# Optimization experiments

Measured on AMD Instinct MI355X. Metric: run time of the kernel, lower is better.

Reference implementation:

```python
import jax, jax.numpy as jnp
import numpy as np

DIM = 768
HEADS = 8
HEAD_DIM = DIM // HEADS  # 96
HIDDEN = 1500
EPS = 1e-5
# Faithful quirk: original divides scores by d = (dim/head_num)**(-0.5)
D_QUIRK = (DIM / HEADS) ** (-0.5)


def setup_inputs() -> dict:
    key = jax.random.key(0)
    ks = jax.random.split(key, 12)
    B, N = 8, 1024
    def lin(k, fan_in, fan_out):
        bound = 1.0 / np.sqrt(fan_in)
        return jax.random.uniform(k, (fan_in, fan_out), jnp.float32, -bound, bound)
    return {
        "x": jax.random.normal(ks[0], (B, N, DIM), jnp.float32),
        "ln_g": jnp.ones((DIM,), jnp.float32),
        "ln_b": jnp.zeros((DIM,), jnp.float32),
        "Wqkv": lin(ks[1], DIM, 3 * DIM),
        "bqkv": jnp.zeros((3 * DIM,), jnp.float32),
        "W0": lin(ks[2], DIM, DIM),
        "b0": jnp.zeros((DIM,), jnp.float32),
        "W1": lin(ks[3], DIM, HIDDEN),
        "b1": jnp.zeros((HIDDEN,), jnp.float32),
        "W2": lin(ks[4], HIDDEN, DIM),
        "b2": jnp.zeros((DIM,), jnp.float32),
    }


def _layer_norm(x, g, b):
    mu = jnp.mean(x, axis=-1, keepdims=True)
    var = jnp.var(x, axis=-1, keepdims=True)
    return (x - mu) * jax.lax.rsqrt(var + EPS) * g + b


def _attention(x, Wqkv, bqkv, W0, b0):
    B, N, C = x.shape
    qkv = x @ Wqkv + bqkv                      # [B,N,3C]
    qkv = qkv.reshape(B, N, 3, HEADS, HEAD_DIM)
    qkv = jnp.transpose(qkv, (2, 0, 3, 1, 4))  # [3,B,H,N,hd]
    q, k, v = qkv[0], qkv[1], qkv[2]
    # Faithful: divide by d = head_dim**(-0.5)  (i.e. multiply by sqrt(head_dim))
    scores = jnp.einsum('bhnd,bhmd->bhnm', q, k) / D_QUIRK
    attn = jax.nn.softmax(scores, axis=-1)
    out = jnp.einsum('bhnm,bhmd->bhnd', attn, v)  # [B,H,N,hd]
    out = jnp.transpose(out, (0, 2, 1, 3)).reshape(B, N, C)
    return out @ W0 + b0


def reference(x, ln_g, ln_b, Wqkv, bqkv, W0, b0, W1, b1, W2, b2):
    y = _layer_norm(x, ln_g, ln_b)
    y = _attention(y, Wqkv, bqkv, W0, b0)
    z = y + x
    k = _layer_norm(z, ln_g, ln_b)  # shared LN params (same module reused)
    k = jax.nn.gelu(k @ W1 + b1, approximate=False) @ W2 + b2
    return z + k
```

## Files before the change

### kernel.cpp

```cpp
#include <hip/hip_runtime.h>
#include <hip/hip_bf16.h>

#define DIM 768
#define HEADS 8
#define HD 96
#define HIDDEN 1500
#define HPAD 1536
#define NB 8
#define NSEQ 1024
#define NTOK (NB * NSEQ)
#define LNEPS 1e-5f
#define ATTN_SCALE 9.797958971132712f

typedef __attribute__((ext_vector_type(4))) float f32x4;
typedef __attribute__((ext_vector_type(8))) __bf16 bf16x8;
typedef __attribute__((ext_vector_type(4))) __bf16 bf16x4;

typedef __attribute__((address_space(1))) const unsigned int GU32;
typedef __attribute__((address_space(3))) unsigned int LU32;

__device__ __forceinline__ void gload16(const void* g, void* l) {
    __builtin_amdgcn_global_load_lds((GU32*)g, (LU32*)l, 16, 0, 0);
}

__device__ __forceinline__ float ldsel(const void* p, size_t i, bool bf) {
    return bf ? __bfloat162float(((const __hip_bfloat16*)p)[i])
              : ((const float*)p)[i];
}

__device__ __forceinline__ float gelu_exact(float x) {
    return 0.5f * x * (1.0f + erff(x * 0.7071067811865476f));
}

__global__ void detect_kernel(const unsigned int* __restrict__ g, int* __restrict__ flag) {
    *flag = (g[0] == 0x3F800000u) ? 0 : 1;
}

template <int INDUAL>
__global__ __launch_bounds__(256) void ln_kernel(const void* __restrict__ x,
                                                 const void* __restrict__ gam,
                                                 const void* __restrict__ bet,
                                                 __bf16* __restrict__ outH,
                                                 __bf16* __restrict__ outL,
                                                 const int* __restrict__ flagp) {
    bool bf = (*flagp != 0);
    int row = blockIdx.x;
    int t = threadIdx.x;
    size_t base = (size_t)row * DIM;
    float v0, v1, v2;
    if (INDUAL) {
        v0 = ldsel(x, base + t, bf);
        v1 = ldsel(x, base + t + 256, bf);
        v2 = ldsel(x, base + t + 512, bf);
    } else {
        const float* xr = (const float*)x + base;
        v0 = xr[t]; v1 = xr[t + 256]; v2 = xr[t + 512];
    }
    float s = v0 + v1 + v2;
    float s2 = v0 * v0 + v1 * v1 + v2 * v2;
    __shared__ float r1[256];
    __shared__ float r2[256];
    r1[t] = s; r2[t] = s2;
    __syncthreads();
    for (int o = 128; o > 0; o >>= 1) {
        if (t < o) { r1[t] += r1[t + o]; r2[t] += r2[t + o]; }
        __syncthreads();
    }
    float mean = r1[0] * (1.0f / DIM);
    float var = r2[0] * (1.0f / DIM) - mean * mean;
    float inv = rsqrtf(var + LNEPS);
    float o0 = (v0 - mean) * inv * ldsel(gam, t, bf)       + ldsel(bet, t, bf);
    float o1 = (v1 - mean) * inv * ldsel(gam, t + 256, bf) + ldsel(bet, t + 256, bf);
    float o2 = (v2 - mean) * inv * ldsel(gam, t + 512, bf) + ldsel(bet, t + 512, bf);
    __bf16 h0 = (__bf16)o0; outH[base + t]       = h0; outL[base + t]       = (__bf16)(o0 - (float)h0);
    __bf16 h1 = (__bf16)o1; outH[base + t + 256] = h1; outL[base + t + 256] = (__bf16)(o1 - (float)h1);
    __bf16 h2 = (__bf16)o2; outH[base + t + 512] = h2; outL[base + t + 512] = (__bf16)(o2 - (float)h2);
}

__global__ __launch_bounds__(256) void wsplit_kernel(const void* __restrict__ W,
                                                     __bf16* __restrict__ WTh,
                                                     __bf16* __restrict__ WTl,
                                                     int K, int N, int Kpad, int Ngrid,
                                                     const int* __restrict__ flagp) {
    bool bf = (*flagp != 0);
    __shared__ float T[32][33];
    int tx = threadIdx.x & 31, ty = threadIdx.x >> 5;
    int k0 = blockIdx.x * 32, n0 = blockIdx.y * 32;
#pragma unroll
    for (int i = 0; i < 4; ++i) {
        int k = k0 + ty + i * 8, n = n0 + tx;
        T[ty + i * 8][tx] = (k < K && n < N) ? ldsel(W, (size_t)k * N + n, bf) : 0.0f;
    }
    __syncthreads();
#pragma unroll
    for (int i = 0; i < 4; ++i) {
        int n = n0 + ty + i * 8, k = k0 + tx;
        if (n < Ngrid && k < Kpad) {
            float v = T[tx][ty + i * 8];
            __bf16 h = (__bf16)v;
            WTh[(size_t)n * Kpad + k] = h;
            WTl[(size_t)n * Kpad + k] = (__bf16)(v - (float)h);
        }
    }
}

template <int ACT, int RES, int OUTMODE>
__global__ __launch_bounds__(256, 2) void gemm_kernel(
    const __bf16* __restrict__ AH, const __bf16* __restrict__ AL,
    const __bf16* __restrict__ BH, const __bf16* __restrict__ BL,
    const void* __restrict__ bias,
    const void* __restrict__ resv, int rstride,
    void* __restrict__ outv, int ostride,
    int K, int Nvalid,
    const int* __restrict__ flagp) {
    bool bf = (*flagp != 0);
    __shared__ __align__(16) __bf16 lds[4 * 8192];
    __bf16* sAH = lds;
    __bf16* sAL = lds + 8192;
    __bf16* sBH = lds + 16384;
    __bf16* sBL = lds + 24576;

    int t = threadIdx.x;
    int lane = t & 63, w = t >> 6;
    int wr = w >> 1, wc = w & 1;
    int lr = lane & 15, kq = lane >> 4;

    int gx = gridDim.x;
    int nwg = gx * gridDim.y;
    int orig = blockIdx.y * gx + blockIdx.x;
    int qq = nwg >> 3, rm = nwg & 7;
    int xcd = orig & 7, loc = orig >> 3;
    int wgid = (xcd < rm ? xcd * (qq + 1) : rm * (qq + 1) + (xcd - rm) * qq) + loc;
    int row0 = (wgid / gx) * 128, col0 = (wgid % gx) * 128;

    size_t asrc[4], bsrc[4];
    int ldst[4];
#pragma unroll
    for (int j = 0; j < 4; ++j) {
        int c = j * 256 + t;
        int rr = c >> 3;
        int kbs = (c & 7) ^ (rr & 7);
        asrc[j] = (size_t)(row0 + rr) * K + kbs * 8;
        bsrc[j] = (size_t)(col0 + rr) * K + kbs * 8;
        ldst[j] = c * 8;
    }

    f32x4 acc[4][4];
#pragma unroll
    for (int mi = 0; mi < 4; ++mi)
#pragma unroll
        for (int ni = 0; ni < 4; ++ni)
            acc[mi][ni] = (f32x4){0.f, 0.f, 0.f, 0.f};

    for (int k0 = 0; k0 < K; k0 += 64) {
        __syncthreads();
#pragma unroll
        for (int j = 0; j < 4; ++j) {
            gload16(AH + asrc[j] + k0, sAH + ldst[j]);
            gload16(AL + asrc[j] + k0, sAL + ldst[j]);
            gload16(BH + bsrc[j] + k0, sBH + ldst[j]);
            gload16(BL + bsrc[j] + k0, sBL + ldst[j]);
        }
        __syncthreads();
#pragma unroll
        for (int s = 0; s < 2; ++s) {
            bf16x8 af_h[4], af_l[4], bt_h[4], bt_l[4];
            int kb = s * 4 + kq;
#pragma unroll
            for (int mi = 0; mi < 4; ++mi) {
                int rowm = wr * 64 + mi * 16 + lr;
                int off = (rowm * 8 + (kb ^ (rowm & 7))) * 8;
                af_h[mi] = *(const bf16x8*)(sAH + off);
                af_l[mi] = *(const bf16x8*)(sAL + off);
            }
#pragma unroll
            for (int ni = 0; ni < 4; ++ni) {
                int rown = wc * 64 + ni * 16 + lr;
                int off = (rown * 8 + (kb ^ (rown & 7))) * 8;
                bt_h[ni] = *(const bf16x8*)(sBH + off);
                bt_l[ni] = *(const bf16x8*)(sBL + off);
            }
            if (!bf) {
#pragma unroll
                for (int mi = 0; mi < 4; ++mi)
#pragma unroll
                    for (int ni = 0; ni < 4; ++ni) {
                        acc[mi][ni] = __builtin_amdgcn_mfma_f32_16x16x32_bf16(af_h[mi], bt_h[ni], acc[mi][ni], 0, 0, 0);
                        acc[mi][ni] = __builtin_amdgcn_mfma_f32_16x16x32_bf16(af_l[mi], bt_h[ni], acc[mi][ni], 0, 0, 0);
                        acc[mi][ni] = __builtin_amdgcn_mfma_f32_16x16x32_bf16(af_h[mi], bt_l[ni], acc[mi][ni], 0, 0, 0);
                    }
            } else {
#pragma unroll
                for (int mi = 0; mi < 4; ++mi)
#pragma unroll
                    for (int ni = 0; ni < 4; ++ni) {
                        acc[mi][ni] = __builtin_amdgcn_mfma_f32_16x16x32_bf16(af_h[mi], bt_h[ni], acc[mi][ni], 0, 0, 0);
                        acc[mi][ni] = __builtin_amdgcn_mfma_f32_16x16x32_bf16(af_l[mi], bt_h[ni], acc[mi][ni], 0, 0, 0);
                    }
            }
        }
    }

    int fr = lane & 15, fq = lane >> 4;
#pragma unroll
    for (int mi = 0; mi < 4; ++mi) {
#pragma unroll
        for (int ni = 0; ni < 4; ++ni) {
            int cc = col0 + wc * 64 + ni * 16 + fr;
#pragma unroll
            for (int j = 0; j < 4; ++j) {
                int rr = row0 + wr * 64 + mi * 16 + fq * 4 + j;
                if (cc < Nvalid) {
                    float cval = acc[mi][ni][j] + ldsel(bias, cc, bf);
                    if (ACT == 1) cval = gelu_exact(cval);
                    if (RES == 1) cval += ldsel(resv, (size_t)rr * rstride + cc, bf);
                    if (RES == 2) cval += ((const float*)resv)[(size_t)rr * rstride + cc];
                    if (OUTMODE == 0) {
                        ((float*)outv)[(size_t)rr * ostride + cc] = cval;
                    } else if (OUTMODE == 1) {
                        if (bf)
                            ((__hip_bfloat16*)outv)[(size_t)rr * ostride + cc] = __float2bfloat16(cval);
                        else
                            ((float*)outv)[(size_t)rr * ostride + cc] = cval;
                    } else {
                        __bf16 hv = (__bf16)cval;
                        ((__bf16*)outv)[(size_t)rr * ostride + cc] = hv;
                        ((__bf16*)outv)[(size_t)NTOK * HPAD + (size_t)rr * ostride + cc] =
                            (__bf16)(cval - (float)hv);
                    }
                } else if (OUTMODE == 2) {
                    ((__bf16*)outv)[(size_t)rr * ostride + cc] = (__bf16)0.0f;
                    ((__bf16*)outv)[(size_t)NTOK * HPAD + (size_t)rr * ostride + cc] = (__bf16)0.0f;
                }
            }
        }
    }
}

__global__ __launch_bounds__(256, 3) void attn_kernel(const float* __restrict__ qkv,
                                                      __bf16* __restrict__ oH,
                                                      __bf16* __restrict__ oL) {
    __shared__ __align__(16) char smem[51200];
    char* Kh_s = smem;
    char* Kl_s = smem + 13312;
    char* Vt_s = smem + 26624;
    char* P_s  = smem + 41984;

    int nwg = gridDim.x * gridDim.y;
    int orig = blockIdx.y * gridDim.x + blockIdx.x;
    int qq = nwg >> 3;
    int wgid = (orig & 7) * qq + (orig >> 3);
    int qt = wgid & 15;
    int bh = wgid >> 4;
    int b = bh >> 3, h = bh & 7;
    int t = threadIdx.x;
    int lane = t & 63, w = t >> 6;
    int r = lane & 15, g = lane >> 4;

    const size_t rs = 3 * DIM;

    bf16x8 qh[3], ql[3];
    {
        const float* qp = qkv + ((size_t)b * NSEQ + qt * 64 + w * 16 + r) * rs + h * HD;
#pragma unroll
        for (int kc = 0; kc < 3; ++kc) {
            f32x4 f0 = *(const f32x4*)(qp + kc * 32 + g * 8);
            f32x4 f1 = *(const f32x4*)(qp + kc * 32 + g * 8 + 4);
#pragma unroll
            for (int j = 0; j < 8; ++j) {
                float f = (j < 4) ? f0[j] : f1[j - 4];
                __bf16 hi = (__bf16)f;
                qh[kc][j] = hi;
                ql[kc][j] = (__bf16)(f - (float)hi);
            }
        }
    }

    f32x4 kreg[6], vreg[8];
    const float* kg0 = qkv + (size_t)b * NSEQ * rs + DIM + h * HD;
    const float* vg0 = qkv + (size_t)b * NSEQ * rs + 2 * DIM + h * HD;
    int vdq = t >> 3, voct = t & 7;

    auto load_kv = [&](int jt) {
        const float* kg = kg0 + (size_t)(jt * 64) * rs;
#pragma unroll
        for (int i = 0; i < 6; ++i) {
            int u = t + i * 256;
            int key = u / 24, dp = u % 24;
            kreg[i] = *(const f32x4*)(kg + (size_t)key * rs + dp * 4);
        }
        if (t < 192) {
            const float* vg = vg0 + (size_t)(jt * 64) * rs;
#pragma unroll
            for (int koff = 0; koff < 8; ++koff)
                vreg[koff] = *(const f32x4*)(vg + (size_t)(voct * 8 + koff) * rs + vdq * 4);
        }
    };

    auto store_kv = [&]() {
#pragma unroll
        for (int i = 0; i < 6; ++i) {
            int u = t + i * 256;
            int key = u / 24, dp = u % 24;
            bf16x4 kh4, kl4;
#pragma unroll
            for (int j = 0; j < 4; ++j) {
                __bf16 hi = (__bf16)kreg[i][j];
                kh4[j] = hi;
                kl4[j] = (__bf16)(kreg[i][j] - (float)hi);
            }
            *(bf16x4*)(Kh_s + key * 208 + dp * 8) = kh4;
            *(bf16x4*)(Kl_s + key * 208 + dp * 8) = kl4;
        }
        if (t < 192) {
#pragma unroll
            for (int j = 0; j < 4; ++j) {
                bf16x8 vrow;
#pragma unroll
                for (int koff = 0; koff < 8; ++koff)
                    vrow[koff] = (__bf16)vreg[koff][j];
                *(bf16x8*)(Vt_s + (vdq * 4 + j) * 160 + voct * 16) = vrow;
            }
        }
    };

    f32x4 o[6];
#pragma unroll
    for (int di = 0; di < 6; ++di) o[di] = (f32x4){0.f, 0.f, 0.f, 0.f};
    float m_i[4], l_i[4];
#pragma unroll
    for (int jj = 0; jj < 4; ++jj) { m_i[jj] = -1e30f; l_i[jj] = 0.0f; }

    load_kv(0);
    for (int jt = 0; jt < NSEQ / 64; ++jt) {
        __syncthreads();
        store_kv();
        __syncthreads();
        if (jt + 1 < NSEQ / 64) load_kv(jt + 1);

        f32x4 sacc[4];
#pragma unroll
        for (int ci = 0; ci < 4; ++ci) sacc[ci] = (f32x4){0.f, 0.f, 0.f, 0.f};
#pragma unroll
        for (int ci = 0; ci < 4; ++ci) {
#pragma unroll
            for (int kc = 0; kc < 3; ++kc) {
                bf16x8 kh = *(const bf16x8*)(Kh_s + (ci * 16 + r) * 208 + kc * 64 + g * 16);
                bf16x8 kl = *(const bf16x8*)(Kl_s + (ci * 16 + r) * 208 + kc * 64 + g * 16);
                sacc[ci] = __builtin_amdgcn_mfma_f32_16x16x32_bf16(qh[kc], kh, sacc[ci], 0, 0, 0);
                sacc[ci] = __builtin_amdgcn_mfma_f32_16x16x32_bf16(ql[kc], kh, sacc[ci], 0, 0, 0);
                sacc[ci] = __builtin_amdgcn_mfma_f32_16x16x32_bf16(qh[kc], kl, sacc[ci], 0, 0, 0);
            }
        }

        float p[4][4];
        float al[4];
#pragma unroll
        for (int jj = 0; jj < 4; ++jj) {
            float s0 = sacc[0][jj] * ATTN_SCALE;
            float s1 = sacc[1][jj] * ATTN_SCALE;
            float s2 = sacc[2][jj] * ATTN_SCALE;
            float s3 = sacc[3][jj] * ATTN_SCALE;
            float mx = fmaxf(fmaxf(s0, s1), fmaxf(s2, s3));
            mx = fmaxf(mx, __shfl_xor(mx, 1));
            mx = fmaxf(mx, __shfl_xor(mx, 2));
            mx = fmaxf(mx, __shfl_xor(mx, 4));
            mx = fmaxf(mx, __shfl_xor(mx, 8));
            float mn = fmaxf(m_i[jj], mx);
            al[jj] = __expf(m_i[jj] - mn);
            p[0][jj] = __expf(s0 - mn);
            p[1][jj] = __expf(s1 - mn);
            p[2][jj] = __expf(s2 - mn);
            p[3][jj] = __expf(s3 - mn);
            float rsm = p[0][jj] + p[1][jj] + p[2][jj] + p[3][jj];
            rsm += __shfl_xor(rsm, 1);
            rsm += __shfl_xor(rsm, 2);
            rsm += __shfl_xor(rsm, 4);
            rsm += __shfl_xor(rsm, 8);
            l_i[jj] = l_i[jj] * al[jj] + rsm;
            m_i[jj] = mn;
        }
#pragma unroll
        for (int di = 0; di < 6; ++di)
#pragma unroll
            for (int jj = 0; jj < 4; ++jj) o[di][jj] *= al[jj];
#pragma unroll
        for (int jj = 0; jj < 4; ++jj)
#pragma unroll
            for (int ci = 0; ci < 4; ++ci)
                ((__bf16*)(P_s + (w * 16 + g * 4 + jj) * 144))[ci * 16 + r] = (__bf16)p[ci][jj];
        asm volatile("" ::: "memory");

        bf16x8 pa[2];
#pragma unroll
        for (int kc2 = 0; kc2 < 2; ++kc2)
            pa[kc2] = *(const bf16x8*)(P_s + (w * 16 + r) * 144 + kc2 * 64 + g * 16);
#pragma unroll
        for (int di = 0; di < 6; ++di) {
#pragma unroll
            for (int kc2 = 0; kc2 < 2; ++kc2) {
                bf16x8 vb = *(const bf16x8*)(Vt_s + (di * 16 + r) * 160 + kc2 * 64 + g * 16);
                o[di] = __builtin_amdgcn_mfma_f32_16x16x32_bf16(pa[kc2], vb, o[di], 0, 0, 0);
            }
        }
    }

    float invl[4];
#pragma unroll
    for (int jj = 0; jj < 4; ++jj) invl[jj] = 1.0f / l_i[jj];
#pragma unroll
    for (int jj = 0; jj < 4; ++jj) {
        size_t tok = (size_t)b * NSEQ + qt * 64 + w * 16 + g * 4 + jj;
        size_t base = tok * DIM + h * HD + r;
#pragma unroll
        for (int di = 0; di < 6; ++di) {
            float v = o[di][jj] * invl[jj];
            __bf16 hv = (__bf16)v;
            oH[base + di * 16] = hv;
            oL[base + di * 16] = (__bf16)(v - (float)hv);
        }
    }
}

extern "C" void kernel_launch(void* const* d_in, const int* in_sizes, int n_in,
                              void* d_out, int out_size, void* d_ws, size_t ws_size,
                              hipStream_t stream) {
    const void* x    = d_in[0];
    const void* ln_g = d_in[1];
    const void* ln_b = d_in[2];
    const void* Wqkv = d_in[3];
    const void* bqkv = d_in[4];
    const void* W0   = d_in[5];
    const void* b0   = d_in[6];
    const void* W1   = d_in[7];
    const void* b1   = d_in[8];
    const void* W2   = d_in[9];
    const void* b2   = d_in[10];

    float* ws = (float*)d_ws;
    __bf16* ylnH = (__bf16*)ws;
    __bf16* ylnL = ylnH + (size_t)NTOK * DIM;
    __bf16* atnH = ylnH;
    __bf16* atnL = ylnL;
    __bf16* klnH = ylnH;
    __bf16* klnL = ylnL;
    float* qkv = ws + (size_t)NTOK * DIM;
    __bf16* r1 = (__bf16*)qkv;
    __bf16* W0Th = r1;
    __bf16* W0Tl = W0Th + (size_t)768 * 768;
    __bf16* W1Th = W0Tl + (size_t)768 * 768;
    __bf16* W1Tl = W1Th + (size_t)HPAD * 768;
    __bf16* W2Th = W1Tl + (size_t)HPAD * 768;
    __bf16* W2Tl = W2Th + (size_t)768 * HPAD;
    __bf16* hH   = W2Tl + (size_t)768 * HPAD;
    __bf16* hL   = hH + (size_t)NTOK * HPAD;
    float* zbuf = ws + (size_t)NTOK * (DIM + 3 * DIM);
    __bf16* WqkvTh = (__bf16*)zbuf;
    __bf16* WqkvTl = WqkvTh + (size_t)(3 * DIM) * DIM;

    int* flag = (int*)(ws + (size_t)NTOK * 3840);

    detect_kernel<<<1, 1, 0, stream>>>((const unsigned int*)ln_g, flag);
    ln_kernel<1><<<NTOK, 256, 0, stream>>>(x, ln_g, ln_b, ylnH, ylnL, flag);
    wsplit_kernel<<<dim3(DIM / 32, (3 * DIM) / 32), 256, 0, stream>>>(
        Wqkv, WqkvTh, WqkvTl, DIM, 3 * DIM, DIM, 3 * DIM, flag);
    gemm_kernel<0, 0, 0><<<dim3((3 * DIM) / 128, NTOK / 128), 256, 0, stream>>>(
        ylnH, ylnL, WqkvTh, WqkvTl, bqkv, nullptr, 0, qkv, 3 * DIM, DIM, 3 * DIM, flag);
    attn_kernel<<<dim3(NSEQ / 64, NB * HEADS), 256, 0, stream>>>(qkv, atnH, atnL);
    wsplit_kernel<<<dim3(DIM / 32, DIM / 32), 256, 0, stream>>>(
        W0, W0Th, W0Tl, DIM, DIM, DIM, DIM, flag);
    wsplit_kernel<<<dim3(DIM / 32, HPAD / 32), 256, 0, stream>>>(
        W1, W1Th, W1Tl, DIM, HIDDEN, DIM, HPAD, flag);
    wsplit_kernel<<<dim3(HPAD / 32, DIM / 32), 256, 0, stream>>>(
        W2, W2Th, W2Tl, HIDDEN, DIM, HPAD, DIM, flag);
    gemm_kernel<0, 1, 0><<<dim3(DIM / 128, NTOK / 128), 256, 0, stream>>>(
        atnH, atnL, W0Th, W0Tl, b0, x, DIM, zbuf, DIM, DIM, DIM, flag);
    ln_kernel<0><<<NTOK, 256, 0, stream>>>(zbuf, ln_g, ln_b, klnH, klnL, flag);
    gemm_kernel<1, 0, 2><<<dim3(HPAD / 128, NTOK / 128), 256, 0, stream>>>(
        klnH, klnL, W1Th, W1Tl, b1, nullptr, 0, hH, HPAD, DIM, HIDDEN, flag);
    gemm_kernel<0, 2, 1><<<dim3(DIM / 128, NTOK / 128), 256, 0, stream>>>(
        hH, hL, W2Th, W2Tl, b2, zbuf, DIM, d_out, DIM, HPAD, DIM, flag);
}
```

Measured before the change: 582.3 us.

## Halve GEMM K-tile, pad V-transpose LDS rows, add lazy softmax rescaling

The GEMM K step drops from 64 to 32 with a new 4-chunk XOR swizzle, halving LDS use per block so more blocks may fit per CU. In attention, the transposed-V row stride grows from 160 to 176 bytes to reduce LDS bank conflicts. The online softmax now rescales the running max and output only when some row's new max exceeds the old one by more than 8, skipping the exponential and multiply work otherwise. In exchange, the GEMM runs twice as many barrier-separated K iterations, and the lazy softmax lets exponentials reach up to e^8 before a rescale, which could overflow bf16 P precision in edge cases.

Result: slower. 655.0 us (+12.5%).

```diff
diff --git a/kernel.cpp b/kernel.cpp
--- a/kernel.cpp
+++ b/kernel.cpp
@@ -114,11 +114,11 @@
     int K, int Nvalid,
     const int* __restrict__ flagp) {
     bool bf = (*flagp != 0);
-    __shared__ __align__(16) __bf16 lds[4 * 8192];
+    __shared__ __align__(16) __bf16 lds[4 * 4096];
     __bf16* sAH = lds;
-    __bf16* sAL = lds + 8192;
-    __bf16* sBH = lds + 16384;
-    __bf16* sBL = lds + 24576;
+    __bf16* sAL = lds + 4096;
+    __bf16* sBH = lds + 8192;
+    __bf16* sBL = lds + 12288;
 
     int t = threadIdx.x;
     int lane = t & 63, w = t >> 6;
@@ -133,13 +133,13 @@
     int wgid = (xcd < rm ? xcd * (qq + 1) : rm * (qq + 1) + (xcd - rm) * qq) + loc;
     int row0 = (wgid / gx) * 128, col0 = (wgid % gx) * 128;
 
-    size_t asrc[4], bsrc[4];
-    int ldst[4];
-#pragma unroll
-    for (int j = 0; j < 4; ++j) {
+    size_t asrc[2], bsrc[2];
+    int ldst[2];
+#pragma unroll
+    for (int j = 0; j < 2; ++j) {
         int c = j * 256 + t;
-        int rr = c >> 3;
-        int kbs = (c & 7) ^ (rr & 7);
+        int rr = c >> 2;
+        int kbs = (c & 3) ^ ((rr >> 1) & 3);
         asrc[j] = (size_t)(row0 + rr) * K + kbs * 8;
         bsrc[j] = (size_t)(col0 + rr) * K + kbs * 8;
         ldst[j] = c * 8;
@@ -152,52 +152,48 @@
         for (int ni = 0; ni < 4; ++ni)
             acc[mi][ni] = (f32x4){0.f, 0.f, 0.f, 0.f};
 
-    for (int k0 = 0; k0 < K; k0 += 64) {
+    for (int k0 = 0; k0 < K; k0 += 32) {
         __syncthreads();
 #pragma unroll
-        for (int j = 0; j < 4; ++j) {
+        for (int j = 0; j < 2; ++j) {
             gload16(AH + asrc[j] + k0, sAH + ldst[j]);
             gload16(AL + asrc[j] + k0, sAL + ldst[j]);
             gload16(BH + bsrc[j] + k0, sBH + ldst[j]);
             gload16(BL + bsrc[j] + k0, sBL + ldst[j]);
         }
         __syncthreads();
-#pragma unroll
-        for (int s = 0; s < 2; ++s) {
-            bf16x8 af_h[4], af_l[4], bt_h[4], bt_l[4];
-            int kb = s * 4 + kq;
-#pragma unroll
-            for (int mi = 0; mi < 4; ++mi) {
-                int rowm = wr * 64 + mi * 16 + lr;
-                int off = (rowm * 8 + (kb ^ (rowm & 7))) * 8;
-                af_h[mi] = *(const bf16x8*)(sAH + off);
-                af_l[mi] = *(const bf16x8*)(sAL + off);
-            }
-#pragma unroll
-            for (int ni = 0; ni < 4; ++ni) {
-                int rown = wc * 64 + ni * 16 + lr;
-                int off = (rown * 8 + (kb ^ (rown & 7))) * 8;
-                bt_h[ni] = *(const bf16x8*)(sBH + off);
-                bt_l[ni] = *(const bf16x8*)(sBL + off);
-            }
-            if (!bf) {
-#pragma unroll
-                for (int mi = 0; mi < 4; ++mi)
-#pragma unroll
-                    for (int ni = 0; ni < 4; ++ni) {
-                        acc[mi][ni] = __builtin_amdgcn_mfma_f32_16x16x32_bf16(af_h[mi], bt_h[ni], acc[mi][ni], 0, 0, 0);
-                        acc[mi][ni] = __builtin_amdgcn_mfma_f32_16x16x32_bf16(af_l[mi], bt_h[ni], acc[mi][ni], 0, 0, 0);
-                        acc[mi][ni] = __builtin_amdgcn_mfma_f32_16x16x32_bf16(af_h[mi], bt_l[ni], acc[mi][ni], 0, 0, 0);
-                    }
-            } else {
-#pragma unroll
-                for (int mi = 0; mi < 4; ++mi)
-#pragma unroll
-                    for (int ni = 0; ni < 4; ++ni) {
-                        acc[mi][ni] = __builtin_amdgcn_mfma_f32_16x16x32_bf16(af_h[mi], bt_h[ni], acc[mi][ni], 0, 0, 0);
-                        acc[mi][ni] = __builtin_amdgcn_mfma_f32_16x16x32_bf16(af_l[mi], bt_h[ni], acc[mi][ni], 0, 0, 0);
-                    }
-            }
+        bf16x8 af_h[4], af_l[4], bt_h[4], bt_l[4];
+#pragma unroll
+        for (int mi = 0; mi < 4; ++mi) {
+            int rowm = wr * 64 + mi * 16 + lr;
+            int off = (rowm * 4 + (kq ^ ((rowm >> 1) & 3))) * 8;
+            af_h[mi] = *(const bf16x8*)(sAH + off);
+            af_l[mi] = *(const bf16x8*)(sAL + off);
+        }
+#pragma unroll
+        for (int ni = 0; ni < 4; ++ni) {
+            int rown = wc * 64 + ni * 16 + lr;
+            int off = (rown * 4 + (kq ^ ((rown >> 1) & 3))) * 8;
+            bt_h[ni] = *(const bf16x8*)(sBH + off);
+            bt_l[ni] = *(const bf16x8*)(sBL + off);
+        }
+        if (!bf) {
+#pragma unroll
+            for (int mi = 0; mi < 4; ++mi)
+#pragma unroll
+                for (int ni = 0; ni < 4; ++ni) {
+                    acc[mi][ni] = __builtin_amdgcn_mfma_f32_16x16x32_bf16(af_h[mi], bt_h[ni], acc[mi][ni], 0, 0, 0);
+                    acc[mi][ni] = __builtin_amdgcn_mfma_f32_16x16x32_bf16(af_l[mi], bt_h[ni], acc[mi][ni], 0, 0, 0);
+                    acc[mi][ni] = __builtin_amdgcn_mfma_f32_16x16x32_bf16(af_h[mi], bt_l[ni], acc[mi][ni], 0, 0, 0);
+                }
+        } else {
+#pragma unroll
+            for (int mi = 0; mi < 4; ++mi)
+#pragma unroll
+                for (int ni = 0; ni < 4; ++ni) {
+                    acc[mi][ni] = __builtin_amdgcn_mfma_f32_16x16x32_bf16(af_h[mi], bt_h[ni], acc[mi][ni], 0, 0, 0);
+                    acc[mi][ni] = __builtin_amdgcn_mfma_f32_16x16x32_bf16(af_l[mi], bt_h[ni], acc[mi][ni], 0, 0, 0);
+                }
         }
     }
 
@@ -240,11 +236,11 @@
 __global__ __launch_bounds__(256, 3) void attn_kernel(const float* __restrict__ qkv,
                                                       __bf16* __restrict__ oH,
                                                       __bf16* __restrict__ oL) {
-    __shared__ __align__(16) char smem[51200];
+    __shared__ __align__(16) char smem[52736];
     char* Kh_s = smem;
     char* Kl_s = smem + 13312;
     char* Vt_s = smem + 26624;
-    char* P_s  = smem + 41984;
+    char* P_s  = smem + 43520;
 
     int nwg = gridDim.x * gridDim.y;
     int orig = blockIdx.y * gridDim.x + blockIdx.x;
@@ -319,7 +315,7 @@
 #pragma unroll
                 for (int koff = 0; koff < 8; ++koff)
                     vrow[koff] = (__bf16)vreg[koff][j];
-                *(bf16x8*)(Vt_s + (vdq * 4 + j) * 160 + voct * 16) = vrow;
+                *(bf16x8*)(Vt_s + (vdq * 4 + j) * 176 + voct * 16) = vrow;
             }
         }
     };
@@ -353,8 +349,8 @@
             }
         }
 
-        float p[4][4];
-        float al[4];
+        float mxj[4];
+        bool grow = false;
 #pragma unroll
         for (int jj = 0; jj < 4; ++jj) {
             float s0 = sacc[0][jj] * ATTN_SCALE;
@@ -366,24 +362,31 @@
             mx = fmaxf(mx, __shfl_xor(mx, 2));
             mx = fmaxf(mx, __shfl_xor(mx, 4));
             mx = fmaxf(mx, __shfl_xor(mx, 8));
-            float mn = fmaxf(m_i[jj], mx);
-            al[jj] = __expf(m_i[jj] - mn);
-            p[0][jj] = __expf(s0 - mn);
-            p[1][jj] = __expf(s1 - mn);
-            p[2][jj] = __expf(s2 - mn);
-            p[3][jj] = __expf(s3 - mn);
+            mxj[jj] = mx;
+            if (mx > m_i[jj] + 8.0f) grow = true;
+        }
+        grow = __any(grow);
+        float p[4][4];
+#pragma unroll
+        for (int jj = 0; jj < 4; ++jj) {
+            float mn = grow ? fmaxf(m_i[jj], mxj[jj]) : m_i[jj];
+            float al = grow ? __expf(m_i[jj] - mn) : 1.0f;
+            p[0][jj] = __expf(sacc[0][jj] * ATTN_SCALE - mn);
+            p[1][jj] = __expf(sacc[1][jj] * ATTN_SCALE - mn);
+            p[2][jj] = __expf(sacc[2][jj] * ATTN_SCALE - mn);
+            p[3][jj] = __expf(sacc[3][jj] * ATTN_SCALE - mn);
             float rsm = p[0][jj] + p[1][jj] + p[2][jj] + p[3][jj];
             rsm += __shfl_xor(rsm, 1);
             rsm += __shfl_xor(rsm, 2);
             rsm += __shfl_xor(rsm, 4);
             rsm += __shfl_xor(rsm, 8);
-            l_i[jj] = l_i[jj] * al[jj] + rsm;
+            l_i[jj] = l_i[jj] * al + rsm;
             m_i[jj] = mn;
-        }
-#pragma unroll
-        for (int di = 0; di < 6; ++di)
-#pragma unroll
-            for (int jj = 0; jj < 4; ++jj) o[di][jj] *= al[jj];
+            if (grow) {
+#pragma unroll
+                for (int di = 0; di < 6; ++di) o[di][jj] *= al;
+            }
+        }
 #pragma unroll
         for (int jj = 0; jj < 4; ++jj)
 #pragma unroll
@@ -399,7 +402,7 @@
         for (int di = 0; di < 6; ++di) {
 #pragma unroll
             for (int kc2 = 0; kc2 < 2; ++kc2) {
-                bf16x8 vb = *(const bf16x8*)(Vt_s + (di * 16 + r) * 160 + kc2 * 64 + g * 16);
+                bf16x8 vb = *(const bf16x8*)(Vt_s + (di * 16 + r) * 176 + kc2 * 64 + g * 16);
                 o[di] = __builtin_amdgcn_mfma_f32_16x16x32_bf16(pa[kc2], vb, o[di], 0, 0, 0);
             }
         }
@@ -410,7 +413,7 @@
     for (int jj = 0; jj < 4; ++jj) invl[jj] = 1.0f / l_i[jj];
 #pragma unroll
     for (int jj = 0; jj < 4; ++jj) {
-        size_t tok = (size_t)b * NSEQ + qt * 64 + w * 16 + g * 4 + jj;
+        size_t tok = (size_t)b * NSEQ + (size_t)qt * 64 + w * 16 + g * 4 + jj;
         size_t base = tok * DIM + h * HD + r;
 #pragma unroll
         for (int di = 0; di < 6; ++di) {
```
